# Kernel optimization log

Measured on AMD Instinct MI355X. Metric: run time of the kernel, lower is better.

## Reference

```python
import jax, jax.numpy as jnp
import numpy as np

NUM_HEADS = 16
ROPE_THETA = 10000.0


def apply_rope(x):
    # x: (B, H, T, hd), interleaved-pair RoPE (rotary-embedding-torch convention)
    T, hd = x.shape[-2], x.shape[-1]
    inv_freq = 1.0 / (ROPE_THETA ** (jnp.arange(0, hd, 2, dtype=jnp.float32) / hd))  # (hd/2,)
    ang = jnp.arange(T, dtype=jnp.float32)[:, None] * inv_freq[None, :]  # (T, hd/2)
    cos, sin = jnp.cos(ang), jnp.sin(ang)
    x1 = x[..., 0::2]
    x2 = x[..., 1::2]
    r1 = x1 * cos - x2 * sin
    r2 = x1 * sin + x2 * cos
    return jnp.stack([r1, r2], axis=-1).reshape(x.shape)


def setup_inputs() -> dict:
    key = jax.random.key(0)
    ks = jax.random.split(key, 8)
    L, S, B, E = 2048, 2048, 2, 1024
    sc = 1.0 / np.sqrt(E)
    return {
        "query": jax.random.normal(ks[0], (L, B, E), jnp.float32),
        "key": jax.random.normal(ks[1], (S, B, E), jnp.float32),
        "value": jax.random.normal(ks[2], (S, B, E), jnp.float32),
        "key_padding_mask": jnp.zeros((B, S), dtype=bool),
        "Wq": jax.random.normal(ks[3], (E, E), jnp.float32) * sc,
        "bq": jnp.zeros((E,), jnp.float32),
        "Wk": jax.random.normal(ks[4], (E, E), jnp.float32) * sc,
        "bk": jnp.zeros((E,), jnp.float32),
        "Wv": jax.random.normal(ks[5], (E, E), jnp.float32) * sc,
        "bv": jnp.zeros((E,), jnp.float32),
        "Wo": jax.random.normal(ks[6], (E, E), jnp.float32) * sc,
        "bo": jnp.zeros((E,), jnp.float32),
    }


def reference(query, key, value, key_padding_mask, Wq, bq, Wk, bk, Wv, bv, Wo, bo):
    L, B, E = query.shape
    S = key.shape[0]
    H = NUM_HEADS
    hd = E // H
    # projections (torch Linear: x @ W.T + b)
    Q = query @ Wq.T + bq  # (L, B, E)
    K = key @ Wk.T + bk    # (S, B, E)
    V = value @ Wv.T + bv  # (S, B, E)
    # (T, B, E) -> (B, H, T, hd)
    Q = Q.reshape(L, B, H, hd).transpose(1, 2, 0, 3)
    K = K.reshape(S, B, H, hd).transpose(1, 2, 0, 3)
    V = V.reshape(S, B, H, hd).transpose(1, 2, 0, 3)
    Q = apply_rope(Q)
    K = apply_rope(K)
    scores = jnp.einsum("bhld,bhsd->bhls", Q, K) / jnp.sqrt(jnp.float32(hd))
    scores = jnp.where(key_padding_mask[:, None, None, :], -jnp.inf, scores)
    attn = jax.nn.softmax(scores, axis=-1)
    out = jnp.einsum("bhls,bhsd->bhld", attn, V)  # (B, H, L, hd)
    out = out.transpose(2, 0, 1, 3).reshape(L, B, E)
    return out @ Wo.T + bo
```

## Files before the change

### kernel.cpp

```cpp
#include <hip/hip_runtime.h>
#include <hip/hip_bf16.h>

typedef __hip_bfloat16 bf16;
typedef short bf16x8 __attribute__((ext_vector_type(8)));
typedef float f32x4 __attribute__((ext_vector_type(4)));
typedef short s4 __attribute__((ext_vector_type(4)));

#define LL 2048
#define SS 2048
#define EE 1024
#define HH 16
#define HD 64
#define MM (LL * 2)

static __device__ __forceinline__ short f2bs(float f) {
  bf16 h = __float2bfloat16(f);
  short u;
  __builtin_memcpy(&u, &h, 2);
  return u;
}

static __device__ __forceinline__ void st8(bf16* p, float4 x, float4 y) {
  bf16x8 v;
  v[0] = f2bs(x.x); v[1] = f2bs(x.y); v[2] = f2bs(x.z); v[3] = f2bs(x.w);
  v[4] = f2bs(y.x); v[5] = f2bs(y.y); v[6] = f2bs(y.z); v[7] = f2bs(y.w);
  *(bf16x8*)p = v;
}

#define GLL16(gp, lp) __builtin_amdgcn_global_load_lds(                        \
    (const __attribute__((address_space(1))) void*)(gp),                       \
    (__attribute__((address_space(3))) void*)(lp), 16, 0, 0)

__global__ __launch_bounds__(256) void tables_kernel(
    float2* __restrict__ tab, const unsigned char* __restrict__ m,
    float* __restrict__ mf) {
  if (blockIdx.x < 256) {
    int i = blockIdx.x * 256 + threadIdx.x;
    int pos = i >> 5, fi = i & 31;
    float freq = expf(-(float)fi * (9.210340371976184f / 32.0f));
    float ang = (float)pos * freq;
    float s, c;
    sincosf(ang, &s, &c);
    tab[i] = make_float2(c, s);
  } else {
    int i = (blockIdx.x - 256) * 256 + threadIdx.x;
    if (i < 2 * SS) mf[i] = m[i] ? -1e30f : 0.f;
  }
}

__global__ __launch_bounds__(256) void cvt4_kernel(
    const float* __restrict__ s0, const float* __restrict__ s1,
    const float* __restrict__ s2, const float* __restrict__ s3,
    bf16* __restrict__ dst) {
  int sel = blockIdx.x >> 10;
  const float* src = (sel == 0) ? s0 : (sel == 1) ? s1 : (sel == 2) ? s2 : s3;
  size_t loc = ((size_t)(blockIdx.x & 1023) * 256 + threadIdx.x) * 4;
  float4 v = *(const float4*)(src + loc);
  s4 p;
  p[0] = f2bs(v.x); p[1] = f2bs(v.y); p[2] = f2bs(v.z); p[3] = f2bs(v.w);
  *(s4*)(dst + (size_t)sel * EE * EE + loc) = p;
}

template<int MODE, bool XB16, bool WB16>
__global__ __launch_bounds__(256) void proj_kernel(
    const void* __restrict__ Xv, const void* __restrict__ Wv,
    const float* __restrict__ bias, void* __restrict__ dstv,
    const float2* __restrict__ tab)
{
  const int w = threadIdx.x >> 6;
  const int lane = threadIdx.x & 63;
  const int l15 = lane & 15, quad = lane >> 4;
  const int tm = blockIdx.x * 128 + w * 32;
  const int tn = blockIdx.y * 64;

  const size_t aoff0 = (size_t)(tm + l15) * EE + quad * 8;
  const size_t aoff1 = aoff0 + (size_t)16 * EE;
  const size_t woff  = (size_t)(tn + l15) * EE + quad * 8;

  f32x4 zero4 = {0.f, 0.f, 0.f, 0.f};
  f32x4 acc[2][4];
#pragma unroll
  for (int mi = 0; mi < 2; ++mi)
#pragma unroll
    for (int ni = 0; ni < 4; ++ni) acc[mi][ni] = zero4;

  for (int k0 = 0; k0 < EE; k0 += 32) {
    bf16x8 a0, a1;
    if (XB16 || MODE == 3) {
      const bf16* Xb = (const bf16*)Xv;
      a0 = *(const bf16x8*)(Xb + aoff0 + k0);
      a1 = *(const bf16x8*)(Xb + aoff1 + k0);
    } else {
      const float* Xf = (const float*)Xv;
#pragma unroll
      for (int j = 0; j < 8; ++j) a0[j] = f2bs(Xf[aoff0 + k0 + j]);
#pragma unroll
      for (int j = 0; j < 8; ++j) a1[j] = f2bs(Xf[aoff1 + k0 + j]);
    }
#pragma unroll
    for (int ni = 0; ni < 4; ++ni) {
      bf16x8 bv;
      if (WB16) {
        const bf16* Wb = (const bf16*)Wv;
        bv = *(const bf16x8*)(Wb + woff + (size_t)ni * 16 * EE + k0);
      } else {
        const float* Wf = (const float*)Wv;
#pragma unroll
        for (int j = 0; j < 8; ++j) bv[j] = f2bs(Wf[woff + (size_t)ni * 16 * EE + k0 + j]);
      }
      acc[0][ni] = __builtin_amdgcn_mfma_f32_16x16x32_bf16(a0, bv, acc[0][ni], 0, 0, 0);
      acc[1][ni] = __builtin_amdgcn_mfma_f32_16x16x32_bf16(a1, bv, acc[1][ni], 0, 0, 0);
    }
  }

  float bz[4];
#pragma unroll
  for (int ni = 0; ni < 4; ++ni) bz[ni] = bias[tn + ni * 16 + l15];

#pragma unroll
  for (int mi = 0; mi < 2; ++mi) {
#pragma unroll
    for (int ni = 0; ni < 4; ++ni) {
      const int n = tn + ni * 16 + l15;
#pragma unroll
      for (int r = 0; r < 4; ++r) {
        const int m = tm + mi * 16 + quad * 4 + r;
        float v = acc[mi][ni][r] + bz[ni];
        if (MODE <= 1) {
          float other = __shfl_xor(v, 1, 64);
          int pos = m >> 1, b = m & 1, d = n & 63, h = n >> 6;
          float2 cs = tab[pos * 32 + (d >> 1)];
          float rv = (d & 1) ? (other * cs.y + v * cs.x) : (v * cs.x - other * cs.y);
          ((bf16*)dstv)[((size_t)(b * HH + h) * LL + pos) * HD + d] = __float2bfloat16(rv);
        } else if (MODE == 2) {
          int pos = m >> 1, b = m & 1, d = n & 63, h = n >> 6;
          ((bf16*)dstv)[((size_t)(b * HH + h) * HD + d) * SS + pos] = __float2bfloat16(v);
        } else {
          ((float*)dstv)[(size_t)m * EE + n] = v;
        }
      }
    }
  }
}

__global__ __launch_bounds__(256, 4) void qkv_kernel(
    const float* __restrict__ Xq, const float* __restrict__ Xk,
    const float* __restrict__ Xv, const bf16* __restrict__ Wb,
    const float* __restrict__ bq, const float* __restrict__ bk,
    const float* __restrict__ bv, bf16* __restrict__ Qr,
    bf16* __restrict__ Kr, bf16* __restrict__ Vt,
    const float2* __restrict__ tab)
{
  __shared__ __align__(16) bf16 As[2][128 * 32];
  __shared__ __align__(16) bf16 Bs[2][64 * 32];

  const int tid = threadIdx.x;
  const int w = tid >> 6;
  const int lane = tid & 63;
  const int l15 = lane & 15, quad = lane >> 4;
  const int id = blockIdx.x;
  const int z = id >> 9;
  const int g = id & 511;
  const int tmb = (g & 31) * 128;
  const int tn  = (g >> 5) * 64;

  const float* Xf = (z == 0) ? Xq : (z == 1) ? Xk : Xv;
  const bf16* Wm  = Wb + (size_t)z * EE * EE;
  const float* bias = (z == 0) ? bq : (z == 1) ? bk : bv;
  bf16* dst = (z == 0) ? Qr : (z == 1) ? Kr : Vt;

  const int ar = tid >> 2;
  const int ac = (tid & 3) * 8;
  const float* gA0 = Xf + (size_t)(tmb + ar) * EE + ac;
  const float* gA1 = gA0 + (size_t)64 * EE;
  const bf16* gB = Wm + (size_t)(tn + w * 16 + (lane >> 2)) * EE + (lane & 3) * 8;

  f32x4 zero4 = {0.f, 0.f, 0.f, 0.f};
  f32x4 acc[2][4];
#pragma unroll
  for (int mi = 0; mi < 2; ++mi)
#pragma unroll
    for (int ni = 0; ni < 4; ++ni) acc[mi][ni] = zero4;

  {
    float4 a00 = *(const float4*)(gA0);
    float4 a01 = *(const float4*)(gA0 + 4);
    float4 a10 = *(const float4*)(gA1);
    float4 a11 = *(const float4*)(gA1 + 4);
    GLL16(gB, (bf16*)&Bs[0][w * 16 * 32] + lane * 8);
    st8(&As[0][ar * 32 + ac], a00, a01);
    st8(&As[0][(64 + ar) * 32 + ac], a10, a11);
  }
  __syncthreads();

  for (int t = 0; t < 32; ++t) {
    const int cur = t & 1;
    float4 a00, a01, a10, a11;
    if (t < 31) {
      const int k0 = (t + 1) * 32;
      a00 = *(const float4*)(gA0 + k0);
      a01 = *(const float4*)(gA0 + k0 + 4);
      a10 = *(const float4*)(gA1 + k0);
      a11 = *(const float4*)(gA1 + k0 + 4);
      GLL16(gB + k0, (bf16*)&Bs[cur ^ 1][w * 16 * 32] + lane * 8);
    }
    bf16x8 af0 = *(const bf16x8*)(&As[cur][(w * 32 + l15) * 32 + quad * 8]);
    bf16x8 af1 = *(const bf16x8*)(&As[cur][(w * 32 + 16 + l15) * 32 + quad * 8]);
#pragma unroll
    for (int ni = 0; ni < 4; ++ni) {
      bf16x8 bfr = *(const bf16x8*)(&Bs[cur][(ni * 16 + l15) * 32 + quad * 8]);
      acc[0][ni] = __builtin_amdgcn_mfma_f32_16x16x32_bf16(af0, bfr, acc[0][ni], 0, 0, 0);
      acc[1][ni] = __builtin_amdgcn_mfma_f32_16x16x32_bf16(af1, bfr, acc[1][ni], 0, 0, 0);
    }
    if (t < 31) {
      st8(&As[cur ^ 1][ar * 32 + ac], a00, a01);
      st8(&As[cur ^ 1][(64 + ar) * 32 + ac], a10, a11);
    }
    __syncthreads();
  }

  float bz[4];
#pragma unroll
  for (int ni = 0; ni < 4; ++ni) bz[ni] = bias[tn + ni * 16 + l15];

#pragma unroll
  for (int mi = 0; mi < 2; ++mi) {
#pragma unroll
    for (int ni = 0; ni < 4; ++ni) {
      const int n = tn + ni * 16 + l15;
#pragma unroll
      for (int r = 0; r < 4; ++r) {
        const int m = tmb + w * 32 + mi * 16 + quad * 4 + r;
        float v = acc[mi][ni][r] + bz[ni];
        if (z <= 1) {
          float other = __shfl_xor(v, 1, 64);
          int pos = m >> 1, b = m & 1, d = n & 63, h = n >> 6;
          float2 cs = tab[pos * 32 + (d >> 1)];
          float rv = (d & 1) ? (other * cs.y + v * cs.x) : (v * cs.x - other * cs.y);
          dst[((size_t)(b * HH + h) * LL + pos) * HD + d] = __float2bfloat16(rv);
        } else {
          int pos = m >> 1, b = m & 1, d = n & 63, h = n >> 6;
          dst[((size_t)(b * HH + h) * HD + d) * SS + pos] = __float2bfloat16(v);
        }
      }
    }
  }
}

__global__ __launch_bounds__(256) void projo_kernel(
    const bf16* __restrict__ X, const bf16* __restrict__ W,
    const float* __restrict__ bias, float* __restrict__ dst)
{
  __shared__ __align__(16) bf16 As[2][64 * 32];
  __shared__ __align__(16) bf16 Bs[2][64 * 32];

  const int tid = threadIdx.x;
  const int w = tid >> 6;
  const int lane = tid & 63;
  const int l15 = lane & 15, quad = lane >> 4;
  const int tmb = blockIdx.x * 64;
  const int tn  = blockIdx.y * 64;

  const bf16* gA = X + (size_t)(tmb + w * 16 + (lane >> 2)) * EE + (lane & 3) * 8;
  const bf16* gB = W + (size_t)(tn  + w * 16 + (lane >> 2)) * EE + (lane & 3) * 8;

  f32x4 zero4 = {0.f, 0.f, 0.f, 0.f};
  f32x4 acc[4];
#pragma unroll
  for (int ni = 0; ni < 4; ++ni) acc[ni] = zero4;

  GLL16(gA, (bf16*)&As[0][w * 16 * 32] + lane * 8);
  GLL16(gB, (bf16*)&Bs[0][w * 16 * 32] + lane * 8);
  __syncthreads();

  for (int t = 0; t < 32; ++t) {
    const int cur = t & 1;
    if (t < 31) {
      const int k0 = (t + 1) * 32;
      GLL16(gA + k0, (bf16*)&As[cur ^ 1][w * 16 * 32] + lane * 8);
      GLL16(gB + k0, (bf16*)&Bs[cur ^ 1][w * 16 * 32] + lane * 8);
    }
    bf16x8 af = *(const bf16x8*)(&As[cur][(w * 16 + l15) * 32 + quad * 8]);
#pragma unroll
    for (int ni = 0; ni < 4; ++ni) {
      bf16x8 bfr = *(const bf16x8*)(&Bs[cur][(ni * 16 + l15) * 32 + quad * 8]);
      acc[ni] = __builtin_amdgcn_mfma_f32_16x16x32_bf16(af, bfr, acc[ni], 0, 0, 0);
    }
    __syncthreads();
  }

  float bz[4];
#pragma unroll
  for (int ni = 0; ni < 4; ++ni) bz[ni] = bias[tn + ni * 16 + l15];

#pragma unroll
  for (int ni = 0; ni < 4; ++ni) {
    const int n = tn + ni * 16 + l15;
#pragma unroll
    for (int r = 0; r < 4; ++r) {
      const int m = tmb + w * 16 + quad * 4 + r;
      dst[(size_t)m * EE + n] = acc[ni][r] + bz[ni];
    }
  }
}

__global__ __launch_bounds__(256) void attn_kernel(
    const bf16* __restrict__ Qr, const bf16* __restrict__ Kr,
    const bf16* __restrict__ Vt, const float* __restrict__ maskf,
    bf16* __restrict__ ctx)
{
  __shared__ __align__(16) bf16 Ks[2][64 * 64];
  __shared__ __align__(16) bf16 Vs[2][64 * 64];
  __shared__ __align__(16) short Plds[4][32][56];

  const int w = threadIdx.x >> 6;
  const int lane = threadIdx.x & 63;
  const int l15 = lane & 15, quad = lane >> 4;
  const int id = blockIdx.x;
  const int bh = id & 31;
  const int qt = id >> 5;
  const int b = bh >> 4, h = bh & 15;
  const int q0 = qt * 128 + w * 32;

  const bf16* Qbh = Qr + (size_t)bh * LL * HD;
  const bf16* Kbh = Kr + (size_t)bh * SS * HD;
  const bf16* Vbh = Vt + (size_t)bh * HD * SS;
  const float* mrow = maskf + b * SS;

  bf16x8 qf[2][2];
#pragma unroll
  for (int mi = 0; mi < 2; ++mi) {
    const bf16* qp = Qbh + (size_t)(q0 + mi * 16 + l15) * HD + quad * 8;
    qf[mi][0] = *(const bf16x8*)(qp);
    qf[mi][1] = *(const bf16x8*)(qp + 32);
  }

  const int srow = lane >> 3;
  const int gswz = ((lane & 7) ^ srow) * 8;
  const int kswz0 = ((quad    ) ^ (l15 & 7)) * 8;
  const int kswz1 = ((quad + 4) ^ (l15 & 7)) * 8;

#define STAGE(buf, S0) {                                                       \
    _Pragma("unroll")                                                          \
    for (int i = 0; i < 2; ++i) {                                              \
      const int rb = w * 16 + i * 8;                                           \
      GLL16(Kbh + (size_t)((S0) + rb + srow) * HD + gswz,                      \
            (bf16*)&Ks[buf][rb * 64] + lane * 8);                              \
      GLL16(Vbh + (size_t)(rb + srow) * SS + (S0) + gswz,                      \
            (bf16*)&Vs[buf][rb * 64] + lane * 8);                              \
    }                                                                          \
  }

  f32x4 zero4 = {0.f, 0.f, 0.f, 0.f};
  f32x4 o[2][4];
#pragma unroll
  for (int mi = 0; mi < 2; ++mi)
#pragma unroll
    for (int t = 0; t < 4; ++t) o[mi][t] = zero4;
  float ps0 = 0.f, ps1 = 0.f;

  STAGE(0, 0);
  __syncthreads();

  for (int t = 0; t < SS / 64; ++t) {
    const int s0 = t * 64;
    const int cur = t & 1;
    if (t + 1 < SS / 64) STAGE(cur ^ 1, s0 + 64);

#pragma unroll
    for (int ss = 0; ss < 2; ++ss) {
      const bf16* Kb = &Ks[cur][ss * 32 * 64];
      bf16x8 kf00 = *(const bf16x8*)(Kb + (l15)      * 64 + kswz0);
      bf16x8 kf01 = *(const bf16x8*)(Kb + (l15)      * 64 + kswz1);
      bf16x8 kf10 = *(const bf16x8*)(Kb + (16 + l15) * 64 + kswz0);
      bf16x8 kf11 = *(const bf16x8*)(Kb + (16 + l15) * 64 + kswz1);
      bf16x8 vf[4];
#pragma unroll
      for (int tt = 0; tt < 4; ++tt)
        vf[tt] = *(const bf16x8*)(&Vs[cur][0] + (tt * 16 + l15) * 64 +
                                  (((ss * 4 + quad) ^ (l15 & 7)) * 8));
      f32x4 mv0 = *(const f32x4*)(mrow + s0 + ss * 32 + quad * 4);
      f32x4 mv1 = *(const f32x4*)(mrow + s0 + ss * 32 + 16 + quad * 4);

#pragma unroll
      for (int mi = 0; mi < 2; ++mi) {
        f32x4 sc0 = zero4, sc1 = zero4;
        sc0 = __builtin_amdgcn_mfma_f32_16x16x32_bf16(kf00, qf[mi][0], sc0, 0, 0, 0);
        sc0 = __builtin_amdgcn_mfma_f32_16x16x32_bf16(kf01, qf[mi][1], sc0, 0, 0, 0);
        sc1 = __builtin_amdgcn_mfma_f32_16x16x32_bf16(kf10, qf[mi][0], sc1, 0, 0, 0);
        sc1 = __builtin_amdgcn_mfma_f32_16x16x32_bf16(kf11, qf[mi][1], sc1, 0, 0, 0);
        s4 pk0, pk1;
#pragma unroll
        for (int r = 0; r < 4; ++r) {
          float p = __expf(sc0[r] * 0.125f + mv0[r]);
          if (mi == 0) ps0 += p; else ps1 += p;
          pk0[r] = f2bs(p);
        }
#pragma unroll
        for (int r = 0; r < 4; ++r) {
          float p = __expf(sc1[r] * 0.125f + mv1[r]);
          if (mi == 0) ps0 += p; else ps1 += p;
          pk1[r] = f2bs(p);
        }
        *(s4*)&Plds[w][mi * 16 + l15][quad * 4] = pk0;
        *(s4*)&Plds[w][mi * 16 + l15][16 + quad * 4] = pk1;
      }
      asm volatile("" ::: "memory");
      bf16x8 pf0 = *(const bf16x8*)&Plds[w][l15][quad * 8];
      bf16x8 pf1 = *(const bf16x8*)&Plds[w][16 + l15][quad * 8];
#pragma unroll
      for (int tt = 0; tt < 4; ++tt) {
        o[0][tt] = __builtin_amdgcn_mfma_f32_16x16x32_bf16(pf0, vf[tt], o[0][tt], 0, 0, 0);
        o[1][tt] = __builtin_amdgcn_mfma_f32_16x16x32_bf16(pf1, vf[tt], o[1][tt], 0, 0, 0);
      }
      asm volatile("" ::: "memory");
    }
    __syncthreads();
  }
#undef STAGE

  float lv0 = ps0; lv0 += __shfl_xor(lv0, 16, 64); lv0 += __shfl_xor(lv0, 32, 64);
  float lv1 = ps1; lv1 += __shfl_xor(lv1, 16, 64); lv1 += __shfl_xor(lv1, 32, 64);

#pragma unroll
  for (int mi = 0; mi < 2; ++mi) {
#pragma unroll
    for (int r = 0; r < 4; ++r) {
      float lv = (mi == 0) ? lv0 : lv1;
      float li = __shfl(lv, quad * 4 + r, 64);
      float inv = 1.0f / li;
      int q = q0 + mi * 16 + quad * 4 + r;
#pragma unroll
      for (int t = 0; t < 4; ++t) {
        float val = o[mi][t][r] * inv;
        ctx[(size_t)(q * 2 + b) * EE + (size_t)h * 64 + t * 16 + l15] = __float2bfloat16(val);
      }
    }
  }
}

extern "C" void kernel_launch(void* const* d_in, const int* in_sizes, int n_in,
                              void* d_out, int out_size, void* d_ws, size_t ws_size,
                              hipStream_t stream) {
  const float* query = (const float*)d_in[0];
  const float* key   = (const float*)d_in[1];
  const float* value = (const float*)d_in[2];
  const unsigned char* mask = (const unsigned char*)d_in[3];
  const float* Wq = (const float*)d_in[4];
  const float* bq = (const float*)d_in[5];
  const float* Wk = (const float*)d_in[6];
  const float* bk = (const float*)d_in[7];
  const float* Wv = (const float*)d_in[8];
  const float* bv = (const float*)d_in[9];
  const float* Wo = (const float*)d_in[10];
  const float* bo = (const float*)d_in[11];

  char* ws = (char*)d_ws;
  const bool big = ws_size >= ((size_t)41 << 20);

  float2* tab   = (float2*)ws;
  float*  maskf = (float*)(ws + (512 << 10));
  bf16* Wb = (bf16*)(ws + ((size_t)1 << 20));
  size_t base = big ? ((size_t)9 << 20) : ((size_t)1 << 20);
  bf16* Qr  = (bf16*)(ws + base);
  bf16* Kr  = (bf16*)(ws + base + ((size_t)8 << 20));
  bf16* Vt  = (bf16*)(ws + base + ((size_t)16 << 20));
  bf16* ctx = (bf16*)(ws + base + ((size_t)24 << 20));

  tables_kernel<<<272, 256, 0, stream>>>(tab, mask, maskf);

  if (big) {
    cvt4_kernel<<<4096, 256, 0, stream>>>(Wq, Wk, Wv, Wo, Wb);
    qkv_kernel<<<1536, 256, 0, stream>>>(query, key, value, Wb, bq, bk, bv,
                                         Qr, Kr, Vt, tab);
  } else {
    dim3 gp(MM / 128, EE / 64);
    proj_kernel<0, false, false><<<gp, 256, 0, stream>>>(query, Wq, bq, Qr, tab);
    proj_kernel<1, false, false><<<gp, 256, 0, stream>>>(key,   Wk, bk, Kr, tab);
    proj_kernel<2, false, false><<<gp, 256, 0, stream>>>(value, Wv, bv, Vt, tab);
  }

  attn_kernel<<<(LL / 128) * 2 * HH, 256, 0, stream>>>(Qr, Kr, Vt, maskf, ctx);

  if (big) {
    dim3 go(MM / 64, EE / 64);
    projo_kernel<<<go, 256, 0, stream>>>(ctx, Wb + (size_t)3 * EE * EE, bo, (float*)d_out);
  } else {
    dim3 gp(MM / 128, EE / 64);
    proj_kernel<3, true, false><<<gp, 256, 0, stream>>>(ctx, Wo, bo, d_out, tab);
  }
}
```

Baseline: 261.7 us.

## Split-K output projection with atomics, fuse prep kernels, raise occupancy hints

Merges the rope/mask table kernel, the weight bf16 conversion and a zero-fill of the output into one prep launch. The output projection is split along K into two halves that accumulate into the zeroed output with float atomicAdd, doubling the block count. Launch bounds are raised on the QKV and output projection kernels to favour occupancy. The atomics add memory traffic and make the summation order nondeterministic, and the zero-fill writes the whole output an extra time.

```diff
diff --git a/kernel.cpp b/kernel.cpp
--- a/kernel.cpp
+++ b/kernel.cpp
@@ -31,34 +31,37 @@
     (const __attribute__((address_space(1))) void*)(gp),                       \
     (__attribute__((address_space(3))) void*)(lp), 16, 0, 0)
 
-__global__ __launch_bounds__(256) void tables_kernel(
+__global__ __launch_bounds__(256) void prep_kernel(
     float2* __restrict__ tab, const unsigned char* __restrict__ m,
-    float* __restrict__ mf) {
-  if (blockIdx.x < 256) {
-    int i = blockIdx.x * 256 + threadIdx.x;
+    float* __restrict__ mf,
+    const float* __restrict__ s0, const float* __restrict__ s1,
+    const float* __restrict__ s2, const float* __restrict__ s3,
+    bf16* __restrict__ wdst, float* __restrict__ zout) {
+  const int bid = blockIdx.x;
+  if (bid < 256) {
+    int i = bid * 256 + threadIdx.x;
     int pos = i >> 5, fi = i & 31;
     float freq = expf(-(float)fi * (9.210340371976184f / 32.0f));
     float ang = (float)pos * freq;
     float s, c;
     sincosf(ang, &s, &c);
     tab[i] = make_float2(c, s);
+  } else if (bid < 272) {
+    int i = (bid - 256) * 256 + threadIdx.x;
+    if (i < 2 * SS) mf[i] = m[i] ? -1e30f : 0.f;
+  } else if (bid < 4368) {
+    int b2 = bid - 272;
+    int sel = b2 >> 10;
+    const float* src = (sel == 0) ? s0 : (sel == 1) ? s1 : (sel == 2) ? s2 : s3;
+    size_t loc = ((size_t)(b2 & 1023) * 256 + threadIdx.x) * 4;
+    float4 v = *(const float4*)(src + loc);
+    s4 p;
+    p[0] = f2bs(v.x); p[1] = f2bs(v.y); p[2] = f2bs(v.z); p[3] = f2bs(v.w);
+    *(s4*)(wdst + (size_t)sel * EE * EE + loc) = p;
   } else {
-    int i = (blockIdx.x - 256) * 256 + threadIdx.x;
-    if (i < 2 * SS) mf[i] = m[i] ? -1e30f : 0.f;
-  }
-}
-
-__global__ __launch_bounds__(256) void cvt4_kernel(
-    const float* __restrict__ s0, const float* __restrict__ s1,
-    const float* __restrict__ s2, const float* __restrict__ s3,
-    bf16* __restrict__ dst) {
-  int sel = blockIdx.x >> 10;
-  const float* src = (sel == 0) ? s0 : (sel == 1) ? s1 : (sel == 2) ? s2 : s3;
-  size_t loc = ((size_t)(blockIdx.x & 1023) * 256 + threadIdx.x) * 4;
-  float4 v = *(const float4*)(src + loc);
-  s4 p;
-  p[0] = f2bs(v.x); p[1] = f2bs(v.y); p[2] = f2bs(v.z); p[3] = f2bs(v.w);
-  *(s4*)(dst + (size_t)sel * EE * EE + loc) = p;
+    size_t i = ((size_t)(bid - 4368) * 256 + threadIdx.x) * 4;
+    *(float4*)(zout + i) = make_float4(0.f, 0.f, 0.f, 0.f);
+  }
 }
 
 template<int MODE, bool XB16, bool WB16>
@@ -143,7 +146,7 @@
   }
 }
 
-__global__ __launch_bounds__(256, 4) void qkv_kernel(
+__global__ __launch_bounds__(256, 6) void qkv_kernel(
     const float* __restrict__ Xq, const float* __restrict__ Xk,
     const float* __restrict__ Xv, const bf16* __restrict__ Wb,
     const float* __restrict__ bq, const float* __restrict__ bk,
@@ -247,7 +250,7 @@
   }
 }
 
-__global__ __launch_bounds__(256) void projo_kernel(
+__global__ __launch_bounds__(256, 8) void projo_kernel(
     const bf16* __restrict__ X, const bf16* __restrict__ W,
     const float* __restrict__ bias, float* __restrict__ dst)
 {
@@ -260,9 +263,10 @@
   const int l15 = lane & 15, quad = lane >> 4;
   const int tmb = blockIdx.x * 64;
   const int tn  = blockIdx.y * 64;
-
-  const bf16* gA = X + (size_t)(tmb + w * 16 + (lane >> 2)) * EE + (lane & 3) * 8;
-  const bf16* gB = W + (size_t)(tn  + w * 16 + (lane >> 2)) * EE + (lane & 3) * 8;
+  const int kb  = blockIdx.z * 512;
+
+  const bf16* gA = X + (size_t)(tmb + w * 16 + (lane >> 2)) * EE + kb + (lane & 3) * 8;
+  const bf16* gB = W + (size_t)(tn  + w * 16 + (lane >> 2)) * EE + kb + (lane & 3) * 8;
 
   f32x4 zero4 = {0.f, 0.f, 0.f, 0.f};
   f32x4 acc[4];
@@ -273,9 +277,9 @@
   GLL16(gB, (bf16*)&Bs[0][w * 16 * 32] + lane * 8);
   __syncthreads();
 
-  for (int t = 0; t < 32; ++t) {
+  for (int t = 0; t < 16; ++t) {
     const int cur = t & 1;
-    if (t < 31) {
+    if (t < 15) {
       const int k0 = (t + 1) * 32;
       GLL16(gA + k0, (bf16*)&As[cur ^ 1][w * 16 * 32] + lane * 8);
       GLL16(gB + k0, (bf16*)&Bs[cur ^ 1][w * 16 * 32] + lane * 8);
@@ -291,7 +295,8 @@
 
   float bz[4];
 #pragma unroll
-  for (int ni = 0; ni < 4; ++ni) bz[ni] = bias[tn + ni * 16 + l15];
+  for (int ni = 0; ni < 4; ++ni)
+    bz[ni] = (blockIdx.z == 0) ? bias[tn + ni * 16 + l15] : 0.f;
 
 #pragma unroll
   for (int ni = 0; ni < 4; ++ni) {
@@ -299,7 +304,7 @@
 #pragma unroll
     for (int r = 0; r < 4; ++r) {
       const int m = tmb + w * 16 + quad * 4 + r;
-      dst[(size_t)m * EE + n] = acc[ni][r] + bz[ni];
+      atomicAdd(&dst[(size_t)m * EE + n], acc[ni][r] + bz[ni]);
     }
   }
 }
@@ -467,10 +472,10 @@
   bf16* Vt  = (bf16*)(ws + base + ((size_t)16 << 20));
   bf16* ctx = (bf16*)(ws + base + ((size_t)24 << 20));
 
-  tables_kernel<<<272, 256, 0, stream>>>(tab, mask, maskf);
+  prep_kernel<<<big ? 8464 : 272, 256, 0, stream>>>(
+      tab, mask, maskf, Wq, Wk, Wv, Wo, Wb, (float*)d_out);
 
   if (big) {
-    cvt4_kernel<<<4096, 256, 0, stream>>>(Wq, Wk, Wv, Wo, Wb);
     qkv_kernel<<<1536, 256, 0, stream>>>(query, key, value, Wb, bq, bk, bv,
                                          Qr, Kr, Vt, tab);
   } else {
@@ -483,7 +488,7 @@
   attn_kernel<<<(LL / 128) * 2 * HH, 256, 0, stream>>>(Qr, Kr, Vt, maskf, ctx);
 
   if (big) {
-    dim3 go(MM / 64, EE / 64);
+    dim3 go(MM / 64, EE / 64, 2);
     projo_kernel<<<go, 256, 0, stream>>>(ctx, Wb + (size_t)3 * EE * EE, bo, (float*)d_out);
   } else {
     dim3 gp(MM / 128, EE / 64);
```

New measurement: 277.5 us. +6.0%, slower.
